# Kernel tuning notes

Measured on AMD Instinct MI355X. Metric: run time of the kernel, lower is better.

Reference implementation:

```python
import jax, jax.numpy as jnp
import numpy as np

B, S, D, H = 2, 2048, 1024, 16
DK = D // H


def setup_inputs() -> dict:
    key = jax.random.key(0)
    ks = jax.random.split(key, 9)
    w_scale = 0.02  # small init for linear weights
    return {
        "query": jax.random.normal(ks[0], (B, S, D), jnp.float32),
        "key": jax.random.normal(ks[1], (B, S, D), jnp.float32),
        "value": jax.random.normal(ks[2], (B, S, D), jnp.float32),
        "mask": jax.random.randint(ks[3], (B, 1, S, S), 0, 2).astype(bool),
        "Wq": jax.random.normal(ks[4], (D, D), jnp.float32) * w_scale,
        "bq": jnp.zeros((D,), jnp.float32),
        "Wk": jax.random.normal(ks[5], (D, D), jnp.float32) * w_scale,
        "bk": jnp.zeros((D,), jnp.float32),
        "Wv": jax.random.normal(ks[6], (D, D), jnp.float32) * w_scale,
        "bv": jnp.zeros((D,), jnp.float32),
        "Wo": jax.random.normal(ks[7], (D, D), jnp.float32) * w_scale,
        "bo": jnp.zeros((D,), jnp.float32),
    }


def _split_heads(x):
    # [B,S,D] -> [B,H,S,DK]
    return x.reshape(B, S, H, DK).transpose(0, 2, 1, 3)


def reference(query, key, value, mask, Wq, bq, Wk, bk, Wv, bv, Wo, bo):
    Q = _split_heads(query @ Wq + bq)
    K = _split_heads(key @ Wk + bk)
    V = _split_heads(value @ Wv + bv)
    scores = jnp.einsum("bhqd,bhkd->bhqk", Q, K) / jnp.sqrt(jnp.float32(DK))
    scores = jnp.where(mask, -jnp.inf, scores)  # masked_fill(mask, -inf)
    attn_w = jax.nn.softmax(scores, axis=-1)
    attn_w = jnp.nan_to_num(attn_w, nan=0.0)  # rows fully masked -> 0
    out = jnp.einsum("bhqk,bhkd->bhqd", attn_w, V)
    out = out.transpose(0, 2, 1, 3).reshape(B, S, D)
    return out @ Wo + bo
```

## Files before the change

kernel.cpp:

```cpp
#include <hip/hip_runtime.h>
#include <hip/hip_bf16.h>
#include <cmath>
#include <cstdint>
#include <cstddef>

#define B_  2
#define S_  2048
#define D_  1024
#define H_  16
#define DK_ 64
#define NEG_BIG (-1e30f)
#define QSCALE 0.1803368801111204f

typedef __attribute__((ext_vector_type(8))) short bf16x8;
typedef __attribute__((ext_vector_type(4))) float f32x4;
typedef __attribute__((ext_vector_type(16))) float f32x16;

static __device__ __forceinline__ unsigned short f2bf(float f) {
  __hip_bfloat16 h = __float2bfloat16(f);
  return *reinterpret_cast<unsigned short*>(&h);
}

static __device__ __forceinline__ unsigned cvtpk(float lo, float hi) {
  unsigned d;
  asm("v_cvt_pk_bf16_f32 %0, %1, %2" : "=v"(d) : "v"(lo), "v"(hi));
  return d;
}
#define SWAP32(a, b) asm("v_permlane32_swap_b32 %0, %1" : "+v"(a), "+v"(b))

typedef __attribute__((address_space(3))) unsigned int lds_u32;
typedef __attribute__((address_space(1))) const unsigned int glb_u32;

__global__ void pack_mask_kernel(const int* __restrict__ mask,
                                 unsigned* __restrict__ bits) {
  const int t = blockIdx.x * 256 + threadIdx.x;
  const unsigned long long ball = __ballot(mask[t] != 0);
  const int lane = threadIdx.x & 63;
  if ((lane & 31) == 0)
    bits[t >> 5] = (lane == 0) ? (unsigned)ball : (unsigned)(ball >> 32);
}

__global__ void cvt_f32_bf16_kernel(const float* __restrict__ q,
                                    const float* __restrict__ k,
                                    const float* __restrict__ v,
                                    unsigned short* __restrict__ qo,
                                    unsigned short* __restrict__ ko,
                                    unsigned short* __restrict__ vo, int n8) {
  int i = blockIdx.x * blockDim.x + threadIdx.x;
  if (i >= n8) return;
  const float* in = (blockIdx.y == 0) ? q : (blockIdx.y == 1) ? k : v;
  unsigned short* out = (blockIdx.y == 0) ? qo : (blockIdx.y == 1) ? ko : vo;
  const float4* p = reinterpret_cast<const float4*>(in) + (size_t)i * 2;
  float4 a = p[0], b = p[1];
  ushort4 o0 = {f2bf(a.x), f2bf(a.y), f2bf(a.z), f2bf(a.w)};
  ushort4 o1 = {f2bf(b.x), f2bf(b.y), f2bf(b.z), f2bf(b.w)};
  ushort4* o = reinterpret_cast<ushort4*>(out) + (size_t)i * 2;
  o[0] = o0;
  o[1] = o1;
}

__global__ __launch_bounds__(256) void transpose_w_kernel(
    const float* __restrict__ w0, const float* __restrict__ w1,
    const float* __restrict__ w2, const float* __restrict__ w3,
    unsigned short* __restrict__ t0, unsigned short* __restrict__ t1,
    unsigned short* __restrict__ t2, unsigned short* __restrict__ t3) {
  __shared__ unsigned short tile[32][33];
  const int z = blockIdx.z;
  const float* W = (z == 0) ? w0 : (z == 1) ? w1 : (z == 2) ? w2 : w3;
  unsigned short* Wt = (z == 0) ? t0 : (z == 1) ? t1 : (z == 2) ? t2 : t3;
  const int r0 = blockIdx.y * 32, c0 = blockIdx.x * 32;
  const int t = threadIdx.x;
  {
    const int r = t >> 3, c4 = (t & 7) * 4;
    float4 v = *reinterpret_cast<const float4*>(&W[(size_t)(r0 + r) * D_ + c0 + c4]);
    tile[c4 + 0][r] = f2bf(v.x);
    tile[c4 + 1][r] = f2bf(v.y);
    tile[c4 + 2][r] = f2bf(v.z);
    tile[c4 + 3][r] = f2bf(v.w);
  }
  __syncthreads();
  {
    const int n = t >> 3, k4 = (t & 7) * 4;
    ushort4 o = {tile[n][k4 + 0], tile[n][k4 + 1], tile[n][k4 + 2], tile[n][k4 + 3]};
    *reinterpret_cast<ushort4*>(&Wt[(size_t)(c0 + n) * D_ + r0 + k4]) = o;
  }
}

__global__ __launch_bounds__(256) void qkv_gemm_kernel(
    const unsigned short* __restrict__ qb, const unsigned short* __restrict__ kb,
    const unsigned short* __restrict__ vb, const unsigned short* __restrict__ wtq,
    const unsigned short* __restrict__ wtk, const unsigned short* __restrict__ wtv,
    const float* __restrict__ bq, const float* __restrict__ bk,
    const float* __restrict__ bv, unsigned short* __restrict__ Qh,
    unsigned short* __restrict__ Kh, unsigned short* __restrict__ VT) {
  constexpr int K = D_;
  __shared__ __attribute__((aligned(16))) unsigned short as_[128 * 32];
  __shared__ __attribute__((aligned(16))) unsigned short bs_[128 * 32];
  const int z = blockIdx.z;
  const unsigned short* A = (z == 0) ? qb : (z == 1) ? kb : vb;
  const unsigned short* Wt = (z == 0) ? wtq : (z == 1) ? wtk : wtv;
  const float* bias = (z == 0) ? bq : (z == 1) ? bk : bv;

  const int bm = blockIdx.x * 128, bn = blockIdx.y * 128;
  const int t = threadIdx.x, wv = t >> 6, lane = t & 63;
  const int r = lane & 15, g = lane >> 4;
  const int wr = (wv >> 1) * 64, wc = (wv & 1) * 64;
  const int srow = 16 * wv + (lane >> 2);
  const int scol = (lane & 3) * 8;

  f32x4 acc[4][4] = {};

  for (int k0 = 0; k0 < K; k0 += 32) {
    __syncthreads();
    __builtin_amdgcn_global_load_lds(
        (glb_u32*)&A[(size_t)(bm + srow) * K + k0 + scol],
        (lds_u32*)(as_ + wv * 512), 16, 0, 0);
    __builtin_amdgcn_global_load_lds(
        (glb_u32*)&A[(size_t)(bm + 64 + srow) * K + k0 + scol],
        (lds_u32*)(as_ + wv * 512 + 2048), 16, 0, 0);
    __builtin_amdgcn_global_load_lds(
        (glb_u32*)&Wt[(size_t)(bn + srow) * K + k0 + scol],
        (lds_u32*)(bs_ + wv * 512), 16, 0, 0);
    __builtin_amdgcn_global_load_lds(
        (glb_u32*)&Wt[(size_t)(bn + 64 + srow) * K + k0 + scol],
        (lds_u32*)(bs_ + wv * 512 + 2048), 16, 0, 0);
    __syncthreads();

    bf16x8 a[4], bfr[4];
#pragma unroll
    for (int mf = 0; mf < 4; ++mf)
      a[mf] = *reinterpret_cast<const bf16x8*>(&as_[(wr + 16 * mf + r) * 32 + 8 * g]);
#pragma unroll
    for (int nf = 0; nf < 4; ++nf)
      bfr[nf] = *reinterpret_cast<const bf16x8*>(&bs_[(wc + 16 * nf + r) * 32 + 8 * g]);
#pragma unroll
    for (int mf = 0; mf < 4; ++mf)
#pragma unroll
      for (int nf = 0; nf < 4; ++nf)
        acc[mf][nf] = __builtin_amdgcn_mfma_f32_16x16x32_bf16(a[mf], bfr[nf],
                                                              acc[mf][nf], 0, 0, 0);
  }

#pragma unroll
  for (int mf = 0; mf < 4; ++mf)
#pragma unroll
    for (int nf = 0; nf < 4; ++nf)
#pragma unroll
      for (int reg = 0; reg < 4; ++reg) {
        const int row = bm + wr + 16 * mf + 4 * g + reg;
        const int col = bn + wc + 16 * nf + r;
        const float v = acc[mf][nf][reg] + bias[col];
        const int bb = row >> 11, s = row & (S_ - 1);
        const int h = col >> 6, dk = col & (DK_ - 1);
        if (z == 0)
          Qh[(((size_t)(bb * H_ + h)) * S_ + s) * DK_ + dk] = f2bf(v * QSCALE);
        else if (z == 1)
          Kh[(((size_t)(bb * H_ + h)) * S_ + s) * DK_ + dk] = f2bf(v);
        else
          VT[(((size_t)(bb * H_ + h)) * DK_ + dk) * S_ + s] = f2bf(v);
      }
}

__global__ __launch_bounds__(256) void out_gemm_kernel(
    const unsigned short* __restrict__ A, const unsigned short* __restrict__ Wt,
    const float* __restrict__ bias, float* __restrict__ Cout) {
  constexpr int K = D_;
  __shared__ __attribute__((aligned(16))) unsigned short as_[128 * 32];
  __shared__ __attribute__((aligned(16))) unsigned short bs_[128 * 32];
  const int bm = blockIdx.x * 128, bn = blockIdx.y * 128;
  const int t = threadIdx.x, wv = t >> 6, lane = t & 63;
  const int r = lane & 15, g = lane >> 4;
  const int wr = (wv >> 1) * 64, wc = (wv & 1) * 64;
  const int srow = 16 * wv + (lane >> 2);
  const int scol = (lane & 3) * 8;

  f32x4 acc[4][4] = {};

  for (int k0 = 0; k0 < K; k0 += 32) {
    __syncthreads();
    __builtin_amdgcn_global_load_lds(
        (glb_u32*)&A[(size_t)(bm + srow) * K + k0 + scol],
        (lds_u32*)(as_ + wv * 512), 16, 0, 0);
    __builtin_amdgcn_global_load_lds(
        (glb_u32*)&A[(size_t)(bm + 64 + srow) * K + k0 + scol],
        (lds_u32*)(as_ + wv * 512 + 2048), 16, 0, 0);
    __builtin_amdgcn_global_load_lds(
        (glb_u32*)&Wt[(size_t)(bn + srow) * K + k0 + scol],
        (lds_u32*)(bs_ + wv * 512), 16, 0, 0);
    __builtin_amdgcn_global_load_lds(
        (glb_u32*)&Wt[(size_t)(bn + 64 + srow) * K + k0 + scol],
        (lds_u32*)(bs_ + wv * 512 + 2048), 16, 0, 0);
    __syncthreads();

    bf16x8 a[4], bfr[4];
#pragma unroll
    for (int mf = 0; mf < 4; ++mf)
      a[mf] = *reinterpret_cast<const bf16x8*>(&as_[(wr + 16 * mf + r) * 32 + 8 * g]);
#pragma unroll
    for (int nf = 0; nf < 4; ++nf)
      bfr[nf] = *reinterpret_cast<const bf16x8*>(&bs_[(wc + 16 * nf + r) * 32 + 8 * g]);
#pragma unroll
    for (int mf = 0; mf < 4; ++mf)
#pragma unroll
      for (int nf = 0; nf < 4; ++nf)
        acc[mf][nf] = __builtin_amdgcn_mfma_f32_16x16x32_bf16(a[mf], bfr[nf],
                                                              acc[mf][nf], 0, 0, 0);
  }

#pragma unroll
  for (int mf = 0; mf < 4; ++mf)
#pragma unroll
    for (int nf = 0; nf < 4; ++nf)
#pragma unroll
      for (int reg = 0; reg < 4; ++reg) {
        const int row = bm + wr + 16 * mf + 4 * g + reg;
        const int col = bn + wc + 16 * nf + r;
        Cout[(size_t)row * D_ + col] = acc[mf][nf][reg] + bias[col];
      }
}

#define ATTN_BODY(KF, KN, PRE)                                                 \
  do {                                                                         \
    const unsigned mw = *mp;                                                   \
    ++mp;                                                                      \
    const bf16x8 vf00 = *(const bf16x8*)(vb0);                                 \
    const bf16x8 vf01 = *(const bf16x8*)(vb0 + 16);                            \
    const bf16x8 vf10 = *(const bf16x8*)(vb1);                                 \
    const bf16x8 vf11 = *(const bf16x8*)(vb1 + 16);                            \
    vb0 += 32;                                                                 \
    vb1 += 32;                                                                 \
    if (PRE) {                                                                 \
      KN[0] = *(const bf16x8*)(kbase);                                         \
      KN[1] = *(const bf16x8*)(kbase + 16);                                    \
      KN[2] = *(const bf16x8*)(kbase + 32);                                    \
      KN[3] = *(const bf16x8*)(kbase + 48);                                    \
      kbase += 2048;                                                           \
    }                                                                          \
    f32x16 sc = {};                                                            \
    sc = __builtin_amdgcn_mfma_f32_32x32x16_bf16(KF[0], qf[0], sc, 0, 0, 0);   \
    sc = __builtin_amdgcn_mfma_f32_32x32x16_bf16(KF[1], qf[1], sc, 0, 0, 0);   \
    sc = __builtin_amdgcn_mfma_f32_32x32x16_bf16(KF[2], qf[2], sc, 0, 0, 0);   \
    sc = __builtin_amdgcn_mfma_f32_32x32x16_bf16(KF[3], qf[3], sc, 0, 0, 0);   \
    const unsigned msh = mw >> (4 * hi);                                       \
    _Pragma("unroll") for (int reg = 0; reg < 16; ++reg) {                     \
      const int creg = (reg & 3) + 8 * (reg >> 2);                             \
      if ((msh >> creg) & 1u) sc[reg] = NEG_BIG;                               \
    }                                                                          \
    float px;                                                                  \
    {                                                                          \
      const float t0 = fmaxf(fmaxf(sc[0], sc[1]), sc[2]);                      \
      const float t1 = fmaxf(fmaxf(sc[3], sc[4]), sc[5]);                      \
      const float t2 = fmaxf(fmaxf(sc[6], sc[7]), sc[8]);                      \
      const float t3 = fmaxf(fmaxf(sc[9], sc[10]), sc[11]);                    \
      const float t4 = fmaxf(fmaxf(sc[12], sc[13]), sc[14]);                   \
      const float u0 = fmaxf(fmaxf(t0, t1), t2);                               \
      const float u1 = fmaxf(fmaxf(t3, t4), sc[15]);                           \
      px = fmaxf(u0, u1);                                                      \
    }                                                                          \
    px = fmaxf(px, __shfl_xor(px, 32));                                        \
    if (!__all(px - m <= 11.f)) {                                              \
      const float mn = fmaxf(m, px);                                           \
      const float al = exp2f(m - mn);                                          \
      m = mn;                                                                  \
      l *= al;                                                                 \
      _Pragma("unroll") for (int reg = 0; reg < 16; ++reg) {                   \
        o0[reg] *= al;                                                         \
        o1[reg] *= al;                                                         \
      }                                                                        \
    }                                                                          \
    _Pragma("unroll") for (int reg = 0; reg < 16; ++reg)                       \
        sc[reg] = exp2f(sc[reg] - m);                                          \
    {                                                                          \
      const float s0 = (sc[0] + sc[1]) + (sc[2] + sc[3]);                      \
      const float s1 = (sc[4] + sc[5]) + (sc[6] + sc[7]);                      \
      const float s2 = (sc[8] + sc[9]) + (sc[10] + sc[11]);                    \
      const float s3 = (sc[12] + sc[13]) + (sc[14] + sc[15]);                  \
      float rs = (s0 + s1) + (s2 + s3);                                        \
      rs += __shfl_xor(rs, 32);                                                \
      l += rs;                                                                 \
    }                                                                          \
    unsigned w0 = cvtpk(sc[0], sc[1]), w2p = cvtpk(sc[4], sc[5]);              \
    unsigned w1 = cvtpk(sc[2], sc[3]), w3p = cvtpk(sc[6], sc[7]);              \
    unsigned u0 = cvtpk(sc[8], sc[9]), u2p = cvtpk(sc[12], sc[13]);            \
    unsigned u1 = cvtpk(sc[10], sc[11]), u3p = cvtpk(sc[14], sc[15]);          \
    SWAP32(w0, w2p);                                                           \
    SWAP32(w1, w3p);                                                           \
    SWAP32(u0, u2p);                                                           \
    SWAP32(u1, u3p);                                                           \
    union { unsigned u[4]; bf16x8 v; } pu0, pu1;                               \
    pu0.u[0] = w0; pu0.u[1] = w1; pu0.u[2] = w2p; pu0.u[3] = w3p;              \
    pu1.u[0] = u0; pu1.u[1] = u1; pu1.u[2] = u2p; pu1.u[3] = u3p;              \
    o0 = __builtin_amdgcn_mfma_f32_32x32x16_bf16(pu0.v, vf00, o0, 0, 0, 0);    \
    o0 = __builtin_amdgcn_mfma_f32_32x32x16_bf16(pu1.v, vf01, o0, 0, 0, 0);    \
    o1 = __builtin_amdgcn_mfma_f32_32x32x16_bf16(pu0.v, vf10, o1, 0, 0, 0);    \
    o1 = __builtin_amdgcn_mfma_f32_32x32x16_bf16(pu1.v, vf11, o1, 0, 0, 0);    \
  } while (0)

__global__ __launch_bounds__(256) void attn_mfma_kernel(
    const unsigned short* __restrict__ Qh, const unsigned short* __restrict__ Kh,
    const unsigned short* __restrict__ VT, const unsigned* __restrict__ mbits,
    unsigned short* __restrict__ ctx) {
  __shared__ float mlds[4][32];
  __shared__ float llds[4][32];
  __shared__ float olds[3][2][16][64];

  const int flat = blockIdx.x;
  const int bh = (flat & 7) * 4 + ((flat >> 3) & 3);
  const int qblk = flat >> 5;
  const int b = bh >> 4, h = bh & 15;
  const int kh = threadIdx.x >> 6, lane = threadIdx.x & 63;
  const int ql = lane & 31, hi = lane >> 5;
  const int qrow = qblk * 32 + ql;

  const unsigned short* Qrow = &Qh[((size_t)bh * S_ + qrow) * DK_];
  bf16x8 qf[4];
#pragma unroll
  for (int i = 0; i < 4; ++i)
    qf[i] = *(const bf16x8*)&Qrow[16 * i + 8 * hi];

  const unsigned short* Khead = &Kh[(size_t)bh * S_ * DK_];
  const unsigned short* Vhead = &VT[(size_t)bh * DK_ * S_];

  f32x16 o0 = {}, o1 = {};
  float m = NEG_BIG, l = 0.f;

  const int tbeg = kh * 16;
  const unsigned short* kbase = Khead + ((size_t)(tbeg * 32 + ql)) * DK_ + 8 * hi;
  const unsigned short* vb0 = Vhead + (size_t)ql * S_ + tbeg * 32 + 8 * hi;
  const unsigned short* vb1 = vb0 + (size_t)32 * S_;
  const unsigned* mp = &mbits[((size_t)b * S_ + qrow) * (S_ / 32) + tbeg];

  bf16x8 kfA[4], kfB[4];
  kfA[0] = *(const bf16x8*)(kbase);
  kfA[1] = *(const bf16x8*)(kbase + 16);
  kfA[2] = *(const bf16x8*)(kbase + 32);
  kfA[3] = *(const bf16x8*)(kbase + 48);
  kbase += 2048;

#pragma unroll 1
  for (int it = 0; it < 7; ++it) {
    ATTN_BODY(kfA, kfB, 1);
    ATTN_BODY(kfB, kfA, 1);
  }
  ATTN_BODY(kfA, kfB, 1);
  ATTN_BODY(kfB, kfA, 0);

  if (lane < 32) {
    mlds[kh][ql] = m;
    llds[kh][ql] = l;
  }
  if (kh < 3) {
#pragma unroll
    for (int reg = 0; reg < 16; ++reg) {
      olds[kh][0][reg][lane] = o0[reg];
      olds[kh][1][reg][lane] = o1[reg];
    }
  }
  __syncthreads();
  if (kh == 3) {
#pragma unroll
    for (int reg = 0; reg < 16; ++reg) {
      const int crow = (reg & 3) + 8 * (reg >> 2) + 4 * hi;
      const float m0 = mlds[0][crow], m1 = mlds[1][crow];
      const float m2 = mlds[2][crow], m3 = mlds[3][crow];
      const float ms = fmaxf(fmaxf(m0, m1), fmaxf(m2, m3));
      const float f0 = exp2f(m0 - ms), f1 = exp2f(m1 - ms);
      const float f2 = exp2f(m2 - ms), f3 = exp2f(m3 - ms);
      const float ls = llds[0][crow] * f0 + llds[1][crow] * f1 +
                       llds[2][crow] * f2 + llds[3][crow] * f3;
      const float inv = (ms == NEG_BIG) ? 0.f : 1.f / ls;
      const float v0 = (olds[0][0][reg][lane] * f0 + olds[1][0][reg][lane] * f1 +
                        olds[2][0][reg][lane] * f2 + o0[reg] * f3) * inv;
      const float v1 = (olds[0][1][reg][lane] * f0 + olds[1][1][reg][lane] * f1 +
                        olds[2][1][reg][lane] * f2 + o1[reg] * f3) * inv;
      const int q = qblk * 32 + crow;
      unsigned short* cp = &ctx[((size_t)(b * S_ + q)) * D_ + h * DK_];
      cp[ql] = f2bf(v0);
      cp[32 + ql] = f2bf(v1);
    }
  }
}

extern "C" void kernel_launch(void* const* d_in, const int* in_sizes, int n_in,
                              void* d_out, int out_size, void* d_ws,
                              size_t ws_size, hipStream_t stream) {
  const float* query = (const float*)d_in[0];
  const float* key   = (const float*)d_in[1];
  const float* value = (const float*)d_in[2];
  const int*   mask  = (const int*)d_in[3];
  const float* Wq = (const float*)d_in[4];
  const float* bq = (const float*)d_in[5];
  const float* Wk = (const float*)d_in[6];
  const float* bk = (const float*)d_in[7];
  const float* Wv = (const float*)d_in[8];
  const float* bv = (const float*)d_in[9];
  const float* Wo = (const float*)d_in[10];
  const float* bo = (const float*)d_in[11];
  float* out = (float*)d_out;

  const size_t nElem = (size_t)B_ * S_ * D_;
  const size_t wElem = (size_t)D_ * D_;
  unsigned short* ws = (unsigned short*)d_ws;
  unsigned short* qb   = ws;
  unsigned short* kb   = qb + nElem;
  unsigned short* vb   = kb + nElem;
  unsigned short* wtq  = vb + nElem;
  unsigned short* wtk  = wtq + wElem;
  unsigned short* wtv  = wtk + wElem;
  unsigned short* wto  = wtv + wElem;
  unsigned short* Qh   = wto + wElem;
  unsigned short* Kh   = Qh + nElem;
  unsigned short* VT   = Kh + nElem;
  unsigned short* ctxb = VT + nElem;
  unsigned* mbits = (unsigned*)(ctxb + nElem);

  pack_mask_kernel<<<(B_ * S_ * S_) / 256, 256, 0, stream>>>(mask, mbits);
  {
    const int n8 = (int)(nElem / 8);
    dim3 grid((n8 + 255) / 256, 3);
    cvt_f32_bf16_kernel<<<grid, 256, 0, stream>>>(query, key, value, qb, kb, vb, n8);
  }
  {
    dim3 grid(32, 32, 4);
    transpose_w_kernel<<<grid, 256, 0, stream>>>(Wq, Wk, Wv, Wo, wtq, wtk, wtv, wto);
  }
  {
    dim3 grid(32, 8, 3);
    qkv_gemm_kernel<<<grid, 256, 0, stream>>>(qb, kb, vb, wtq, wtk, wtv,
                                              bq, bk, bv, Qh, Kh, VT);
  }
  attn_mfma_kernel<<<2048, 256, 0, stream>>>(Qh, Kh, VT, mbits, ctxb);
  {
    dim3 grid(32, 8);
    out_gemm_kernel<<<grid, 256, 0, stream>>>(ctxb, wto, bo, out);
  }
}
```

Before: 352.1 us.

## Fuse input bf16 conversion into QKV GEMM and widen attention KV step

Removes the standalone f32→bf16 conversion kernel. The QKV GEMM now loads fp32 activations directly, converts them in registers with packed cvt, and writes bf16 tiles to LDS. This drops one launch and a full round trip of the activations through memory, but the A-tile load becomes a register-staged load instead of the async global-to-LDS copy. Separately, the attention inner loop now handles 64 keys per iteration with two score tiles, sharing one max/rescale step per pair, and uses raw v_exp_f32 instead of exp2f.

```diff
diff --git a/kernel.cpp b/kernel.cpp
--- a/kernel.cpp
+++ b/kernel.cpp
@@ -26,6 +26,11 @@
   asm("v_cvt_pk_bf16_f32 %0, %1, %2" : "=v"(d) : "v"(lo), "v"(hi));
   return d;
 }
+static __device__ __forceinline__ float vexp2(float x) {
+  float r;
+  asm("v_exp_f32 %0, %1" : "=v"(r) : "v"(x));
+  return r;
+}
 #define SWAP32(a, b) asm("v_permlane32_swap_b32 %0, %1" : "+v"(a), "+v"(b))
 
 typedef __attribute__((address_space(3))) unsigned int lds_u32;
@@ -38,25 +43,6 @@
   const int lane = threadIdx.x & 63;
   if ((lane & 31) == 0)
     bits[t >> 5] = (lane == 0) ? (unsigned)ball : (unsigned)(ball >> 32);
-}
-
-__global__ void cvt_f32_bf16_kernel(const float* __restrict__ q,
-                                    const float* __restrict__ k,
-                                    const float* __restrict__ v,
-                                    unsigned short* __restrict__ qo,
-                                    unsigned short* __restrict__ ko,
-                                    unsigned short* __restrict__ vo, int n8) {
-  int i = blockIdx.x * blockDim.x + threadIdx.x;
-  if (i >= n8) return;
-  const float* in = (blockIdx.y == 0) ? q : (blockIdx.y == 1) ? k : v;
-  unsigned short* out = (blockIdx.y == 0) ? qo : (blockIdx.y == 1) ? ko : vo;
-  const float4* p = reinterpret_cast<const float4*>(in) + (size_t)i * 2;
-  float4 a = p[0], b = p[1];
-  ushort4 o0 = {f2bf(a.x), f2bf(a.y), f2bf(a.z), f2bf(a.w)};
-  ushort4 o1 = {f2bf(b.x), f2bf(b.y), f2bf(b.z), f2bf(b.w)};
-  ushort4* o = reinterpret_cast<ushort4*>(out) + (size_t)i * 2;
-  o[0] = o0;
-  o[1] = o1;
 }
 
 __global__ __launch_bounds__(256) void transpose_w_kernel(
@@ -87,8 +73,8 @@
 }
 
 __global__ __launch_bounds__(256) void qkv_gemm_kernel(
-    const unsigned short* __restrict__ qb, const unsigned short* __restrict__ kb,
-    const unsigned short* __restrict__ vb, const unsigned short* __restrict__ wtq,
+    const float* __restrict__ qa, const float* __restrict__ ka,
+    const float* __restrict__ va, const unsigned short* __restrict__ wtq,
     const unsigned short* __restrict__ wtk, const unsigned short* __restrict__ wtv,
     const float* __restrict__ bq, const float* __restrict__ bk,
     const float* __restrict__ bv, unsigned short* __restrict__ Qh,
@@ -97,7 +83,7 @@
   __shared__ __attribute__((aligned(16))) unsigned short as_[128 * 32];
   __shared__ __attribute__((aligned(16))) unsigned short bs_[128 * 32];
   const int z = blockIdx.z;
-  const unsigned short* A = (z == 0) ? qb : (z == 1) ? kb : vb;
+  const float* A = (z == 0) ? qa : (z == 1) ? ka : va;
   const unsigned short* Wt = (z == 0) ? wtq : (z == 1) ? wtk : wtv;
   const float* bias = (z == 0) ? bq : (z == 1) ? bk : bv;
 
@@ -107,23 +93,30 @@
   const int wr = (wv >> 1) * 64, wc = (wv & 1) * 64;
   const int srow = 16 * wv + (lane >> 2);
   const int scol = (lane & 3) * 8;
+  const int ar0 = t >> 2, ak0 = (t & 3) * 8;
+  const int ar1 = (t + 256) >> 2, ak1 = ak0;
 
   f32x4 acc[4][4] = {};
 
   for (int k0 = 0; k0 < K; k0 += 32) {
+    const float4* ap0 = reinterpret_cast<const float4*>(&A[(size_t)(bm + ar0) * K + k0 + ak0]);
+    const float4* ap1 = reinterpret_cast<const float4*>(&A[(size_t)(bm + ar1) * K + k0 + ak1]);
+    float4 a0 = ap0[0], a1 = ap0[1];
+    float4 a2 = ap1[0], a3 = ap1[1];
     __syncthreads();
-    __builtin_amdgcn_global_load_lds(
-        (glb_u32*)&A[(size_t)(bm + srow) * K + k0 + scol],
-        (lds_u32*)(as_ + wv * 512), 16, 0, 0);
-    __builtin_amdgcn_global_load_lds(
-        (glb_u32*)&A[(size_t)(bm + 64 + srow) * K + k0 + scol],
-        (lds_u32*)(as_ + wv * 512 + 2048), 16, 0, 0);
     __builtin_amdgcn_global_load_lds(
         (glb_u32*)&Wt[(size_t)(bn + srow) * K + k0 + scol],
         (lds_u32*)(bs_ + wv * 512), 16, 0, 0);
     __builtin_amdgcn_global_load_lds(
         (glb_u32*)&Wt[(size_t)(bn + 64 + srow) * K + k0 + scol],
         (lds_u32*)(bs_ + wv * 512 + 2048), 16, 0, 0);
+    union { unsigned u[4]; bf16x8 v; } w0, w1;
+    w0.u[0] = cvtpk(a0.x, a0.y); w0.u[1] = cvtpk(a0.z, a0.w);
+    w0.u[2] = cvtpk(a1.x, a1.y); w0.u[3] = cvtpk(a1.z, a1.w);
+    w1.u[0] = cvtpk(a2.x, a2.y); w1.u[1] = cvtpk(a2.z, a2.w);
+    w1.u[2] = cvtpk(a3.x, a3.y); w1.u[3] = cvtpk(a3.z, a3.w);
+    *reinterpret_cast<bf16x8*>(&as_[(size_t)t * 8]) = w0.v;
+    *reinterpret_cast<bf16x8*>(&as_[(size_t)(t + 256) * 8]) = w1.v;
     __syncthreads();
 
     bf16x8 a[4], bfr[4];
@@ -219,83 +212,6 @@
       }
 }
 
-#define ATTN_BODY(KF, KN, PRE)                                                 \
-  do {                                                                         \
-    const unsigned mw = *mp;                                                   \
-    ++mp;                                                                      \
-    const bf16x8 vf00 = *(const bf16x8*)(vb0);                                 \
-    const bf16x8 vf01 = *(const bf16x8*)(vb0 + 16);                            \
-    const bf16x8 vf10 = *(const bf16x8*)(vb1);                                 \
-    const bf16x8 vf11 = *(const bf16x8*)(vb1 + 16);                            \
-    vb0 += 32;                                                                 \
-    vb1 += 32;                                                                 \
-    if (PRE) {                                                                 \
-      KN[0] = *(const bf16x8*)(kbase);                                         \
-      KN[1] = *(const bf16x8*)(kbase + 16);                                    \
-      KN[2] = *(const bf16x8*)(kbase + 32);                                    \
-      KN[3] = *(const bf16x8*)(kbase + 48);                                    \
-      kbase += 2048;                                                           \
-    }                                                                          \
-    f32x16 sc = {};                                                            \
-    sc = __builtin_amdgcn_mfma_f32_32x32x16_bf16(KF[0], qf[0], sc, 0, 0, 0);   \
-    sc = __builtin_amdgcn_mfma_f32_32x32x16_bf16(KF[1], qf[1], sc, 0, 0, 0);   \
-    sc = __builtin_amdgcn_mfma_f32_32x32x16_bf16(KF[2], qf[2], sc, 0, 0, 0);   \
-    sc = __builtin_amdgcn_mfma_f32_32x32x16_bf16(KF[3], qf[3], sc, 0, 0, 0);   \
-    const unsigned msh = mw >> (4 * hi);                                       \
-    _Pragma("unroll") for (int reg = 0; reg < 16; ++reg) {                     \
-      const int creg = (reg & 3) + 8 * (reg >> 2);                             \
-      if ((msh >> creg) & 1u) sc[reg] = NEG_BIG;                               \
-    }                                                                          \
-    float px;                                                                  \
-    {                                                                          \
-      const float t0 = fmaxf(fmaxf(sc[0], sc[1]), sc[2]);                      \
-      const float t1 = fmaxf(fmaxf(sc[3], sc[4]), sc[5]);                      \
-      const float t2 = fmaxf(fmaxf(sc[6], sc[7]), sc[8]);                      \
-      const float t3 = fmaxf(fmaxf(sc[9], sc[10]), sc[11]);                    \
-      const float t4 = fmaxf(fmaxf(sc[12], sc[13]), sc[14]);                   \
-      const float u0 = fmaxf(fmaxf(t0, t1), t2);                               \
-      const float u1 = fmaxf(fmaxf(t3, t4), sc[15]);                           \
-      px = fmaxf(u0, u1);                                                      \
-    }                                                                          \
-    px = fmaxf(px, __shfl_xor(px, 32));                                        \
-    if (!__all(px - m <= 11.f)) {                                              \
-      const float mn = fmaxf(m, px);                                           \
-      const float al = exp2f(m - mn);                                          \
-      m = mn;                                                                  \
-      l *= al;                                                                 \
-      _Pragma("unroll") for (int reg = 0; reg < 16; ++reg) {                   \
-        o0[reg] *= al;                                                         \
-        o1[reg] *= al;                                                         \
-      }                                                                        \
-    }                                                                          \
-    _Pragma("unroll") for (int reg = 0; reg < 16; ++reg)                       \
-        sc[reg] = exp2f(sc[reg] - m);                                          \
-    {                                                                          \
-      const float s0 = (sc[0] + sc[1]) + (sc[2] + sc[3]);                      \
-      const float s1 = (sc[4] + sc[5]) + (sc[6] + sc[7]);                      \
-      const float s2 = (sc[8] + sc[9]) + (sc[10] + sc[11]);                    \
-      const float s3 = (sc[12] + sc[13]) + (sc[14] + sc[15]);                  \
-      float rs = (s0 + s1) + (s2 + s3);                                        \
-      rs += __shfl_xor(rs, 32);                                                \
-      l += rs;                                                                 \
-    }                                                                          \
-    unsigned w0 = cvtpk(sc[0], sc[1]), w2p = cvtpk(sc[4], sc[5]);              \
-    unsigned w1 = cvtpk(sc[2], sc[3]), w3p = cvtpk(sc[6], sc[7]);              \
-    unsigned u0 = cvtpk(sc[8], sc[9]), u2p = cvtpk(sc[12], sc[13]);            \
-    unsigned u1 = cvtpk(sc[10], sc[11]), u3p = cvtpk(sc[14], sc[15]);          \
-    SWAP32(w0, w2p);                                                           \
-    SWAP32(w1, w3p);                                                           \
-    SWAP32(u0, u2p);                                                           \
-    SWAP32(u1, u3p);                                                           \
-    union { unsigned u[4]; bf16x8 v; } pu0, pu1;                               \
-    pu0.u[0] = w0; pu0.u[1] = w1; pu0.u[2] = w2p; pu0.u[3] = w3p;              \
-    pu1.u[0] = u0; pu1.u[1] = u1; pu1.u[2] = u2p; pu1.u[3] = u3p;              \
-    o0 = __builtin_amdgcn_mfma_f32_32x32x16_bf16(pu0.v, vf00, o0, 0, 0, 0);    \
-    o0 = __builtin_amdgcn_mfma_f32_32x32x16_bf16(pu1.v, vf01, o0, 0, 0, 0);    \
-    o1 = __builtin_amdgcn_mfma_f32_32x32x16_bf16(pu0.v, vf10, o1, 0, 0, 0);    \
-    o1 = __builtin_amdgcn_mfma_f32_32x32x16_bf16(pu1.v, vf11, o1, 0, 0, 0);    \
-  } while (0)
-
 __global__ __launch_bounds__(256) void attn_mfma_kernel(
     const unsigned short* __restrict__ Qh, const unsigned short* __restrict__ Kh,
     const unsigned short* __restrict__ VT, const unsigned* __restrict__ mbits,
@@ -324,26 +240,131 @@
   f32x16 o0 = {}, o1 = {};
   float m = NEG_BIG, l = 0.f;
 
-  const int tbeg = kh * 16;
-  const unsigned short* kbase = Khead + ((size_t)(tbeg * 32 + ql)) * DK_ + 8 * hi;
-  const unsigned short* vb0 = Vhead + (size_t)ql * S_ + tbeg * 32 + 8 * hi;
+  const unsigned short* kbase = Khead + ((size_t)(kh * 512 + ql)) * DK_ + 8 * hi;
+  const unsigned short* vb0 = Vhead + (size_t)ql * S_ + kh * 512 + 8 * hi;
   const unsigned short* vb1 = vb0 + (size_t)32 * S_;
-  const unsigned* mp = &mbits[((size_t)b * S_ + qrow) * (S_ / 32) + tbeg];
-
-  bf16x8 kfA[4], kfB[4];
-  kfA[0] = *(const bf16x8*)(kbase);
-  kfA[1] = *(const bf16x8*)(kbase + 16);
-  kfA[2] = *(const bf16x8*)(kbase + 32);
-  kfA[3] = *(const bf16x8*)(kbase + 48);
-  kbase += 2048;
+  const unsigned* mp = &mbits[((size_t)b * S_ + qrow) * (S_ / 32) + kh * 16];
+
+  bf16x8 kc0[4], kc1[4];
+#pragma unroll
+  for (int i = 0; i < 4; ++i) {
+    kc0[i] = *(const bf16x8*)(kbase + 16 * i);
+    kc1[i] = *(const bf16x8*)(kbase + 2048 + 16 * i);
+  }
+  kbase += 4096;
 
 #pragma unroll 1
-  for (int it = 0; it < 7; ++it) {
-    ATTN_BODY(kfA, kfB, 1);
-    ATTN_BODY(kfB, kfA, 1);
-  }
-  ATTN_BODY(kfA, kfB, 1);
-  ATTN_BODY(kfB, kfA, 0);
+  for (int it = 0; it < 8; ++it) {
+    const uint2 mw = *reinterpret_cast<const uint2*>(mp);
+    mp += 2;
+    bf16x8 vf0[4], vf1[4];
+#pragma unroll
+    for (int kk = 0; kk < 4; ++kk) {
+      vf0[kk] = *(const bf16x8*)(vb0 + kk * 16);
+      vf1[kk] = *(const bf16x8*)(vb1 + kk * 16);
+    }
+    vb0 += 64;
+    vb1 += 64;
+
+    f32x16 sc0 = {}, sc1 = {};
+#pragma unroll
+    for (int i = 0; i < 4; ++i)
+      sc0 = __builtin_amdgcn_mfma_f32_32x32x16_bf16(kc0[i], qf[i], sc0, 0, 0, 0);
+#pragma unroll
+    for (int i = 0; i < 4; ++i)
+      sc1 = __builtin_amdgcn_mfma_f32_32x32x16_bf16(kc1[i], qf[i], sc1, 0, 0, 0);
+
+    if (it < 7) {
+#pragma unroll
+      for (int i = 0; i < 4; ++i) {
+        kc0[i] = *(const bf16x8*)(kbase + 16 * i);
+        kc1[i] = *(const bf16x8*)(kbase + 2048 + 16 * i);
+      }
+      kbase += 4096;
+    }
+
+    const unsigned m0 = mw.x >> (4 * hi), m1 = mw.y >> (4 * hi);
+#pragma unroll
+    for (int reg = 0; reg < 16; ++reg) {
+      const int creg = (reg & 3) + 8 * (reg >> 2);
+      if ((m0 >> creg) & 1u) sc0[reg] = NEG_BIG;
+      if ((m1 >> creg) & 1u) sc1[reg] = NEG_BIG;
+    }
+
+    float px;
+    {
+      float t0 = fmaxf(fmaxf(sc0[0], sc0[1]), sc0[2]);
+      float t1 = fmaxf(fmaxf(sc0[3], sc0[4]), sc0[5]);
+      float t2 = fmaxf(fmaxf(sc0[6], sc0[7]), sc0[8]);
+      float t3 = fmaxf(fmaxf(sc0[9], sc0[10]), sc0[11]);
+      float t4 = fmaxf(fmaxf(sc0[12], sc0[13]), sc0[14]);
+      float t5 = fmaxf(fmaxf(sc0[15], sc1[0]), sc1[1]);
+      float t6 = fmaxf(fmaxf(sc1[2], sc1[3]), sc1[4]);
+      float t7 = fmaxf(fmaxf(sc1[5], sc1[6]), sc1[7]);
+      float t8 = fmaxf(fmaxf(sc1[8], sc1[9]), sc1[10]);
+      float t9 = fmaxf(fmaxf(sc1[11], sc1[12]), sc1[13]);
+      float ta = fmaxf(sc1[14], sc1[15]);
+      float u0 = fmaxf(fmaxf(t0, t1), t2);
+      float u1 = fmaxf(fmaxf(t3, t4), t5);
+      float u2 = fmaxf(fmaxf(t6, t7), t8);
+      float u3 = fmaxf(t9, ta);
+      px = fmaxf(fmaxf(u0, u1), fmaxf(u2, u3));
+    }
+    px = fmaxf(px, __shfl_xor(px, 32));
+
+    if (!__all(px - m <= 11.f)) {
+      const float mn = fmaxf(m, px);
+      const float al = vexp2(m - mn);
+      m = mn;
+      l *= al;
+#pragma unroll
+      for (int reg = 0; reg < 16; ++reg) { o0[reg] *= al; o1[reg] *= al; }
+    }
+
+#pragma unroll
+    for (int reg = 0; reg < 16; ++reg) {
+      sc0[reg] = vexp2(sc0[reg] - m);
+      sc1[reg] = vexp2(sc1[reg] - m);
+    }
+    {
+      float s0 = (sc0[0] + sc0[1]) + (sc0[2] + sc0[3]);
+      float s1 = (sc0[4] + sc0[5]) + (sc0[6] + sc0[7]);
+      float s2 = (sc0[8] + sc0[9]) + (sc0[10] + sc0[11]);
+      float s3 = (sc0[12] + sc0[13]) + (sc0[14] + sc0[15]);
+      float s4 = (sc1[0] + sc1[1]) + (sc1[2] + sc1[3]);
+      float s5 = (sc1[4] + sc1[5]) + (sc1[6] + sc1[7]);
+      float s6 = (sc1[8] + sc1[9]) + (sc1[10] + sc1[11]);
+      float s7 = (sc1[12] + sc1[13]) + (sc1[14] + sc1[15]);
+      float rs = ((s0 + s1) + (s2 + s3)) + ((s4 + s5) + (s6 + s7));
+      rs += __shfl_xor(rs, 32);
+      l += rs;
+    }
+
+    unsigned w0 = cvtpk(sc0[0], sc0[1]), w2p = cvtpk(sc0[4], sc0[5]);
+    unsigned w1 = cvtpk(sc0[2], sc0[3]), w3p = cvtpk(sc0[6], sc0[7]);
+    unsigned x0 = cvtpk(sc0[8], sc0[9]), x2p = cvtpk(sc0[12], sc0[13]);
+    unsigned x1 = cvtpk(sc0[10], sc0[11]), x3p = cvtpk(sc0[14], sc0[15]);
+    unsigned y0 = cvtpk(sc1[0], sc1[1]), y2p = cvtpk(sc1[4], sc1[5]);
+    unsigned y1 = cvtpk(sc1[2], sc1[3]), y3p = cvtpk(sc1[6], sc1[7]);
+    unsigned z0 = cvtpk(sc1[8], sc1[9]), z2p = cvtpk(sc1[12], sc1[13]);
+    unsigned z1 = cvtpk(sc1[10], sc1[11]), z3p = cvtpk(sc1[14], sc1[15]);
+    SWAP32(w0, w2p); SWAP32(w1, w3p); SWAP32(x0, x2p); SWAP32(x1, x3p);
+    SWAP32(y0, y2p); SWAP32(y1, y3p); SWAP32(z0, z2p); SWAP32(z1, z3p);
+    union { unsigned u[4]; bf16x8 v; } pu0, pu1, pu2, pu3;
+    pu0.u[0] = w0; pu0.u[1] = w1; pu0.u[2] = w2p; pu0.u[3] = w3p;
+    pu1.u[0] = x0; pu1.u[1] = x1; pu1.u[2] = x2p; pu1.u[3] = x3p;
+    pu2.u[0] = y0; pu2.u[1] = y1; pu2.u[2] = y2p; pu2.u[3] = y3p;
+    pu3.u[0] = z0; pu3.u[1] = z1; pu3.u[2] = z2p; pu3.u[3] = z3p;
+
+    o0 = __builtin_amdgcn_mfma_f32_32x32x16_bf16(pu0.v, vf0[0], o0, 0, 0, 0);
+    o0 = __builtin_amdgcn_mfma_f32_32x32x16_bf16(pu1.v, vf0[1], o0, 0, 0, 0);
+    o0 = __builtin_amdgcn_mfma_f32_32x32x16_bf16(pu2.v, vf0[2], o0, 0, 0, 0);
+    o0 = __builtin_amdgcn_mfma_f32_32x32x16_bf16(pu3.v, vf0[3], o0, 0, 0, 0);
+    o1 = __builtin_amdgcn_mfma_f32_32x32x16_bf16(pu0.v, vf1[0], o1, 0, 0, 0);
+    o1 = __builtin_amdgcn_mfma_f32_32x32x16_bf16(pu1.v, vf1[1], o1, 0, 0, 0);
+    o1 = __builtin_amdgcn_mfma_f32_32x32x16_bf16(pu2.v, vf1[2], o1, 0, 0, 0);
+    o1 = __builtin_amdgcn_mfma_f32_32x32x16_bf16(pu3.v, vf1[3], o1, 0, 0, 0);
+  }
 
   if (lane < 32) {
     mlds[kh][ql] = m;
@@ -364,8 +385,8 @@
       const float m0 = mlds[0][crow], m1 = mlds[1][crow];
       const float m2 = mlds[2][crow], m3 = mlds[3][crow];
       const float ms = fmaxf(fmaxf(m0, m1), fmaxf(m2, m3));
-      const float f0 = exp2f(m0 - ms), f1 = exp2f(m1 - ms);
-      const float f2 = exp2f(m2 - ms), f3 = exp2f(m3 - ms);
+      const float f0 = vexp2(m0 - ms), f1 = vexp2(m1 - ms);
+      const float f2 = vexp2(m2 - ms), f3 = vexp2(m3 - ms);
       const float ls = llds[0][crow] * f0 + llds[1][crow] * f1 +
                        llds[2][crow] * f2 + llds[3][crow] * f3;
       const float inv = (ms == NEG_BIG) ? 0.f : 1.f / ls;
@@ -401,10 +422,7 @@
   const size_t nElem = (size_t)B_ * S_ * D_;
   const size_t wElem = (size_t)D_ * D_;
   unsigned short* ws = (unsigned short*)d_ws;
-  unsigned short* qb   = ws;
-  unsigned short* kb   = qb + nElem;
-  unsigned short* vb   = kb + nElem;
-  unsigned short* wtq  = vb + nElem;
+  unsigned short* wtq  = ws;
   unsigned short* wtk  = wtq + wElem;
   unsigned short* wtv  = wtk + wElem;
   unsigned short* wto  = wtv + wElem;
@@ -416,17 +434,12 @@
 
   pack_mask_kernel<<<(B_ * S_ * S_) / 256, 256, 0, stream>>>(mask, mbits);
   {
-    const int n8 = (int)(nElem / 8);
-    dim3 grid((n8 + 255) / 256, 3);
-    cvt_f32_bf16_kernel<<<grid, 256, 0, stream>>>(query, key, value, qb, kb, vb, n8);
-  }
-  {
     dim3 grid(32, 32, 4);
     transpose_w_kernel<<<grid, 256, 0, stream>>>(Wq, Wk, Wv, Wo, wtq, wtk, wtv, wto);
   }
   {
     dim3 grid(32, 8, 3);
-    qkv_gemm_kernel<<<grid, 256, 0, stream>>>(qb, kb, vb, wtq, wtk, wtv,
+    qkv_gemm_kernel<<<grid, 256, 0, stream>>>(query, key, value, wtq, wtk, wtv,
                                               bq, bk, bv, Qh, Kh, VT);
   }
   attn_mfma_kernel<<<2048, 256, 0, stream>>>(Qh, Kh, VT, mbits, ctxb);
```

Result: no change. 354.2 us (+0.6%).
